# Performance work log

Hardware: AMD Instinct MI355X
Metric: run time of the kernel (lower is better)

## Reference

```python
import jax, jax.numpy as jnp
import numpy as np

B, S, D, H, EXPAND = 4, 2048, 256, 4, 4
DH = D // H
EPS = 1e-3  # keras BatchNormalization default epsilon
NEG = -1e9  # keras Softmax masking constant


def setup_inputs() -> dict:
    key = jax.random.key(0)
    ks = jax.random.split(key, 8)
    x = jax.random.normal(ks[0], (B, S, D), dtype=jnp.float32)
    mask = jax.random.randint(ks[1], (B, S), 0, 2) > 0
    mask = mask.at[:, 0].set(True)  # ensure each row has a valid token
    sc = 1.0 / np.sqrt(D)
    return {
        "x": x,
        "mask": mask,
        "bn1_gamma": jnp.ones((D,), jnp.float32),
        "bn1_beta": jnp.zeros((D,), jnp.float32),
        "bn1_mean": jax.random.normal(ks[2], (D,), jnp.float32) * 0.1,
        "bn1_var": jnp.ones((D,), jnp.float32),
        "qkv_w": jax.random.normal(ks[3], (D, 3 * D), jnp.float32) * sc,
        "proj_w": jax.random.normal(ks[4], (D, D), jnp.float32) * sc,
        "bn2_gamma": jnp.ones((D,), jnp.float32),
        "bn2_beta": jnp.zeros((D,), jnp.float32),
        "bn2_mean": jax.random.normal(ks[5], (D,), jnp.float32) * 0.1,
        "bn2_var": jnp.ones((D,), jnp.float32),
        "w1": jax.random.normal(ks[6], (D, EXPAND * D), jnp.float32) * sc,
        "w2": jax.random.normal(ks[7], (EXPAND * D, D), jnp.float32) * (sc / 2.0),
    }


def _bn(x, gamma, beta, mean, var):
    # inference-mode BatchNormalization over the channel axis
    return (x - mean) * jax.lax.rsqrt(var + EPS) * gamma + beta


def reference(x, mask, bn1_gamma, bn1_beta, bn1_mean, bn1_var, qkv_w, proj_w,
              bn2_gamma, bn2_beta, bn2_mean, bn2_var, w1, w2):
    scale = D ** (-0.5)
    # --- attention sub-block ---
    skip = x
    h = _bn(x, bn1_gamma, bn1_beta, bn1_mean, bn1_var)
    qkv = h @ qkv_w                                    # [B,S,3D]
    qkv = qkv.reshape(B, S, H, 3 * DH).transpose(0, 2, 1, 3)  # [B,H,S,3dh]
    q, k, v = qkv[..., :DH], qkv[..., DH:2 * DH], qkv[..., 2 * DH:]
    scores = jnp.einsum('bhqd,bhkd->bhqk', q, k) * scale      # [B,H,S,S]
    scores = scores + jnp.where(mask[:, None, None, :], 0.0, NEG)
    attn = jax.nn.softmax(scores, axis=-1)
    o = jnp.einsum('bhqk,bhkd->bhqd', attn, v)                # [B,H,S,dh]
    o = o.transpose(0, 2, 1, 3).reshape(B, S, D) @ proj_w
    x = o + skip
    # --- FFN sub-block ---
    skip = x
    h = _bn(x, bn2_gamma, bn2_beta, bn2_mean, bn2_var)
    h = jax.nn.swish(h @ w1)                                  # [B,S,4D]
    h = h @ w2
    return h + skip
```

## Files before the change

kernel.cpp:

```cpp
#include <hip/hip_runtime.h>
#include <math.h>

#define S_ 2048
#define D_ 256
#define B_ 4
#define H_ 4

typedef __attribute__((ext_vector_type(8))) short  bh8;
typedef __attribute__((ext_vector_type(4))) float  fx4;
typedef __attribute__((ext_vector_type(4))) unsigned short us4;
typedef __attribute__((ext_vector_type(4))) unsigned int   ux4;

__device__ inline unsigned short bf16r(float f) {
    unsigned int u = __builtin_bit_cast(unsigned int, f);
    return (unsigned short)((u + 0x7FFFu + ((u >> 16) & 1u)) >> 16);
}
__device__ inline unsigned int cvtpk(float a, float b) {
    unsigned int r;
    asm("v_cvt_pk_bf16_f32 %0, %1, %2" : "=v"(r) : "v"(a), "v"(b));
    return r;
}
__device__ inline float vexp2(float x) {
    float r;
    asm volatile("v_exp_f32 %0, %1\n\ts_nop 1" : "=v"(r) : "v"(x));
    return r;
}
__device__ inline void gl_lds16(const unsigned short* g, unsigned short* l) {
    __builtin_amdgcn_global_load_lds(
        (const __attribute__((address_space(1))) unsigned int*)g,
        (__attribute__((address_space(3))) unsigned int*)l, 16, 0, 0);
}
#define DRAIN_BARRIER() asm volatile("s_waitcnt vmcnt(0)\n\ts_barrier" ::: "memory")

__global__ __launch_bounds__(256) void prep_all_k(
    const float* __restrict__ qkv_w, const float* __restrict__ proj_w,
    const float* __restrict__ w1,    const float* __restrict__ w2,
    unsigned short* __restrict__ qkv_wt, unsigned short* __restrict__ proj_wt,
    unsigned short* __restrict__ w1t,    unsigned short* __restrict__ w2t,
    const float* __restrict__ x,
    const float* __restrict__ g1, const float* __restrict__ b1,
    const float* __restrict__ m1, const float* __restrict__ v1,
    unsigned short* __restrict__ xb,
    const int* __restrict__ mask, float* __restrict__ maskf)
{
    const int bidx = blockIdx.x;
    if (bidx < 768) {
        const float* W; unsigned short* Wt; int K, N, u0;
        if (bidx < 192)      { W = qkv_w;  Wt = qkv_wt;  K = 256;  N = 768;  u0 = bidx * 256; }
        else if (bidx < 256) { W = proj_w; Wt = proj_wt; K = 256;  N = 256;  u0 = (bidx - 192) * 256; }
        else if (bidx < 512) { W = w1;     Wt = w1t;     K = 256;  N = 1024; u0 = (bidx - 256) * 256; }
        else                 { W = w2;     Wt = w2t;     K = 1024; N = 256;  u0 = (bidx - 512) * 256; }
        const int u = u0 + threadIdx.x;
        const int k4 = u / N, n = u % N;
        us4 tv;
        #pragma unroll
        for (int j = 0; j < 4; ++j) tv[j] = bf16r(W[(size_t)(k4 * 4 + j) * N + n]);
        *(us4*)&Wt[(size_t)n * K + k4 * 4] = tv;
    } else if (bidx < 2816) {
        const int i = (bidx - 768) * 256 + threadIdx.x;
        const int c4 = (i & 63) * 4;
        float4 xv = *(const float4*)&x[(size_t)i * 4];
        float vv[4] = {xv.x, xv.y, xv.z, xv.w};
        us4 tv;
        #pragma unroll
        for (int j = 0; j < 4; ++j) {
            int c = c4 + j;
            float s = g1[c] * rsqrtf(v1[c] + 1e-3f);
            tv[j] = bf16r(vv[j] * s + (b1[c] - m1[c] * s));
        }
        *(us4*)&xb[(size_t)i * 4] = tv;
    } else {
        const int i = (bidx - 2816) * 256 + threadIdx.x;
        maskf[i] = mask[i] ? 0.0f : -1e9f;
    }
}

template<int BM, int E>
__global__ __launch_bounds__(256) void gemm_mfma_k(
    const unsigned short* __restrict__ A, const unsigned short* __restrict__ Wt,
    int N, int K,
    const float* __restrict__ res, float* __restrict__ outf,
    unsigned short* __restrict__ outb, unsigned short* __restrict__ kf_o,
    unsigned short* __restrict__ vf_o,
    const float* __restrict__ g2, const float* __restrict__ b2,
    const float* __restrict__ m2, const float* __restrict__ v2)
{
    constexpr int MI = BM / 32;
    constexpr int LA = BM / 32;
    __shared__ unsigned short Asb[2][BM * 64];
    __shared__ unsigned short Bsb[2][128 * 64];

    const int n0 = blockIdx.x * 128, m0 = blockIdx.y * BM;
    const int t = threadIdx.x, w = t >> 6, l = t & 63;
    const int qi = l & 15, g = l >> 4;
    const int wm = w >> 1, wn = w & 1;
    const int lr = l >> 3, lc = (l & 7) * 8;

    fx4 acc[MI][4];
    #pragma unroll
    for (int mi = 0; mi < MI; ++mi)
        #pragma unroll
        for (int ni = 0; ni < 4; ++ni) acc[mi][ni] = (fx4){0.f, 0.f, 0.f, 0.f};

    const int NT = K / 64;

#define STAGE(P, KT) {                                                        \
    const int kb = (KT) * 64;                                                 \
    _Pragma("unroll")                                                         \
    for (int i = 0; i < LA; ++i) {                                            \
        int r0 = (w * LA + i) * 8;                                            \
        gl_lds16(A + (size_t)(m0 + r0 + lr) * K + kb + lc, &Asb[P][r0 * 64]); \
    }                                                                         \
    _Pragma("unroll")                                                         \
    for (int i = 0; i < 4; ++i) {                                             \
        int r0 = (w * 4 + i) * 8;                                             \
        gl_lds16(Wt + (size_t)(n0 + r0 + lr) * K + kb + lc, &Bsb[P][r0 * 64]);\
    } }

    STAGE(0, 0);
    DRAIN_BARRIER();
    int p = 0;
    for (int kt = 0; kt < NT; ++kt) {
        if (kt + 1 < NT) STAGE(p ^ 1, kt + 1);
        #pragma unroll
        for (int kk = 0; kk < 2; ++kk) {
            bh8 af[MI], bf[4];
            #pragma unroll
            for (int mi = 0; mi < MI; ++mi)
                af[mi] = *(const bh8*)&Asb[p][(wm * (BM / 2) + mi * 16 + qi) * 64
                                             + kk * 32 + g * 8];
            #pragma unroll
            for (int ni = 0; ni < 4; ++ni)
                bf[ni] = *(const bh8*)&Bsb[p][(wn * 64 + ni * 16 + qi) * 64
                                             + kk * 32 + g * 8];
            #pragma unroll
            for (int mi = 0; mi < MI; ++mi)
                #pragma unroll
                for (int ni = 0; ni < 4; ++ni)
                    acc[mi][ni] = __builtin_amdgcn_mfma_f32_16x16x32_bf16(
                        af[mi], bf[ni], acc[mi][ni], 0, 0, 0);
        }
        DRAIN_BARRIER();
        p ^= 1;
    }
#undef STAGE

    const int mbase = m0 + wm * (BM / 2);
    #pragma unroll
    for (int ni = 0; ni < 4; ++ni) {
        const int nf = n0 + wn * 64 + ni * 16;
        if (E == 0) {
            const int h = nf / 192, rem = nf % 192;
            const int region = rem / 64;
            const int c = rem % 64 + qi;
            #pragma unroll
            for (int mi = 0; mi < MI; ++mi) {
                #pragma unroll
                for (int r = 0; r < 4; ++r) {
                    const int m = mbase + mi * 16 + g * 4 + r;
                    const int s = m & 2047;
                    const size_t bh = (size_t)((m >> 11) * 4 + h);
                    float a = acc[mi][ni][r];
                    if (region < 2) {
                        size_t off = (((bh * 128 + (s >> 4)) * 2 + (c >> 5)) * 64
                                      + ((c >> 3) & 3) * 16 + (s & 15)) * 8 + (c & 7);
                        if (region == 0)
                            outb[off] = bf16r(a * (0.0625f * 1.44269504f));
                        else
                            kf_o[off] = bf16r(a);
                    } else {
                        size_t off = ((((bh * 32 + (s >> 6)) * 4 + (c >> 4)) * 2
                                      + ((s >> 5) & 1)) * 64
                                      + ((s >> 3) & 3) * 16 + (c & 15)) * 8 + (s & 7);
                        vf_o[off] = bf16r(a);
                    }
                }
            }
        } else if (E == 1) {
            const int n = nf + qi;
            const float s2 = g2[n] * rsqrtf(v2[n] + 1e-3f);
            const float o2 = b2[n] - m2[n] * s2;
            #pragma unroll
            for (int mi = 0; mi < MI; ++mi) {
                #pragma unroll
                for (int r = 0; r < 4; ++r) {
                    const int m = mbase + mi * 16 + g * 4 + r;
                    const size_t idx = (size_t)m * N + n;
                    float rv = acc[mi][ni][r] + res[idx];
                    outf[idx] = rv;
                    outb[idx] = bf16r(rv * s2 + o2);
                }
            }
        } else if (E == 2) {
            const int n = nf + qi;
            #pragma unroll
            for (int mi = 0; mi < MI; ++mi) {
                #pragma unroll
                for (int r = 0; r < 4; ++r) {
                    const int m = mbase + mi * 16 + g * 4 + r;
                    float a = acc[mi][ni][r];
                    outb[(size_t)m * N + n] = bf16r(a / (1.0f + __expf(-a)));
                }
            }
        } else {
            const int n = nf + qi;
            #pragma unroll
            for (int mi = 0; mi < MI; ++mi) {
                #pragma unroll
                for (int r = 0; r < 4; ++r) {
                    const int m = mbase + mi * 16 + g * 4 + r;
                    const size_t idx = (size_t)m * N + n;
                    outf[idx] = acc[mi][ni][r] + res[idx];
                }
            }
        }
    }
}

__global__ __launch_bounds__(256) void attn_mfma_k(
    const unsigned short* __restrict__ qf,
    const unsigned short* __restrict__ kf,
    const unsigned short* __restrict__ vf,
    const float* __restrict__ maskf,
    unsigned short* __restrict__ ob)
{
    __shared__ fx4  Ol[2][64][4];
    __shared__ float Ll[2][64];

    const int bid = blockIdx.x;
    const int bh = bid & 15, qt = bid >> 4;
    const int b = bh >> 2, h = bh & 3;
    const int t = threadIdx.x;
    const int w = t >> 6, lane = t & 63;
    const int g = lane >> 4, qi = lane & 15;
    const int qsub = qt * 2 + (w & 1);
    const int khalf = w >> 1;

    bh8 qf0, qf1;
    {
        const unsigned short* qp =
            qf + (size_t)((bh * 128 + qsub) * 2) * 512 + lane * 8;
        qf0 = *(const bh8*)(qp);
        qf1 = *(const bh8*)(qp + 512);
    }

    fx4 o[4];
    #pragma unroll
    for (int dt = 0; dt < 4; ++dt) o[dt] = (fx4){0.f, 0.f, 0.f, 0.f};
    float lsum = 0.f;

    const unsigned short* kcur = kf + (size_t)bh * 131072 + khalf * 65536 + lane * 8;
    const unsigned short* vcur = vf + (size_t)bh * 131072 + khalf * 65536 + lane * 8;
    const float* mcur = maskf + b * 2048 + khalf * 1024 + g * 4;

    bh8 kfA[4][2], kfB[4][2], afA[4][2], afB[4][2];
    fx4 mvA[4], mvB[4];

#define LOADK(KF, MV) {                                                       \
    KF[0][0] = *(const bh8*)(kcur);        KF[0][1] = *(const bh8*)(kcur + 512);  \
    KF[1][0] = *(const bh8*)(kcur + 1024); KF[1][1] = *(const bh8*)(kcur + 1536); \
    KF[2][0] = *(const bh8*)(kcur + 2048); KF[2][1] = *(const bh8*)(kcur + 2560); \
    KF[3][0] = *(const bh8*)(kcur + 3072); KF[3][1] = *(const bh8*)(kcur + 3584); \
    MV[0] = *(const fx4*)(mcur);      MV[1] = *(const fx4*)(mcur + 16);       \
    MV[2] = *(const fx4*)(mcur + 32); MV[3] = *(const fx4*)(mcur + 48);       \
    kcur += 4096; mcur += 64; }

#define LOADV(AF) {                                                           \
    AF[0][0] = *(const bh8*)(vcur);        AF[0][1] = *(const bh8*)(vcur + 512);  \
    AF[1][0] = *(const bh8*)(vcur + 1024); AF[1][1] = *(const bh8*)(vcur + 1536); \
    AF[2][0] = *(const bh8*)(vcur + 2048); AF[2][1] = *(const bh8*)(vcur + 2560); \
    AF[3][0] = *(const bh8*)(vcur + 3072); AF[3][1] = *(const bh8*)(vcur + 3584); \
    vcur += 4096; }

#define PROCESS(KF, AF, MV) {                                                 \
    fx4 s[4];                                                                 \
    _Pragma("unroll")                                                         \
    for (int kt = 0; kt < 4; ++kt) {                                          \
        fx4 z = MV[kt];                                                       \
        z = __builtin_amdgcn_mfma_f32_16x16x32_bf16(KF[kt][0], qf0, z, 0, 0, 0); \
        z = __builtin_amdgcn_mfma_f32_16x16x32_bf16(KF[kt][1], qf1, z, 0, 0, 0); \
        s[kt] = z;                                                            \
    }                                                                         \
    unsigned int pkv[4][2];                                                   \
    _Pragma("unroll")                                                         \
    for (int kt = 0; kt < 4; ++kt) {                                          \
        float p0 = vexp2(s[kt][0]);                                           \
        float p1 = vexp2(s[kt][1]);                                           \
        float p2 = vexp2(s[kt][2]);                                           \
        float p3 = vexp2(s[kt][3]);                                           \
        lsum += (p0 + p1) + (p2 + p3);                                        \
        pkv[kt][0] = cvtpk(p0, p1);                                           \
        pkv[kt][1] = cvtpk(p2, p3);                                           \
    }                                                                         \
    _Pragma("unroll")                                                         \
    for (int c = 0; c < 2; ++c) {                                             \
        unsigned int bw[4];                                                   \
        _Pragma("unroll")                                                     \
        for (int wd = 0; wd < 4; ++wd) {                                      \
            int src = (2 * (g & 1) + (wd >> 1)) * 16 + qi;                    \
            unsigned int va = (unsigned int)__shfl((int)pkv[2 * c][wd & 1], src, 64);     \
            unsigned int vb = (unsigned int)__shfl((int)pkv[2 * c + 1][wd & 1], src, 64); \
            bw[wd] = (g >= 2) ? vb : va;                                      \
        }                                                                     \
        ux4 bwv = (ux4){bw[0], bw[1], bw[2], bw[3]};                          \
        bh8 bfrag = __builtin_bit_cast(bh8, bwv);                             \
        _Pragma("unroll")                                                     \
        for (int dt = 0; dt < 4; ++dt)                                        \
            o[dt] = __builtin_amdgcn_mfma_f32_16x16x32_bf16(                  \
                AF[dt][c], bfrag, o[dt], 0, 0, 0);                            \
    } }

    LOADK(kfA, mvA);
    LOADV(afA);
    for (int it = 0; it < 16; it += 2) {
        LOADK(kfB, mvB);
        LOADV(afB);
        PROCESS(kfA, afA, mvA);
        if (it + 2 < 16) {
            LOADK(kfA, mvA);
            LOADV(afA);
        }
        PROCESS(kfB, afB, mvB);
    }
#undef LOADK
#undef LOADV
#undef PROCESS

    const int pair = w & 1;
    if (w >= 2) {
        #pragma unroll
        for (int dt = 0; dt < 4; ++dt) Ol[pair][lane][dt] = o[dt];
        Ll[pair][lane] = lsum;
    }
    __syncthreads();
    if (w < 2) {
        lsum += Ll[pair][lane];
        #pragma unroll
        for (int dt = 0; dt < 4; ++dt) {
            fx4 ov = Ol[pair][lane][dt];
            o[dt][0] += ov[0]; o[dt][1] += ov[1];
            o[dt][2] += ov[2]; o[dt][3] += ov[3];
        }
        lsum += __shfl_xor(lsum, 16, 64);
        lsum += __shfl_xor(lsum, 32, 64);
        float inv = 1.0f / lsum;
        unsigned short* op =
            ob + (size_t)(b * 2048 + qsub * 16 + qi) * 256 + h * 64 + g * 4;
        #pragma unroll
        for (int dt = 0; dt < 4; ++dt) {
            us4 tv;
            #pragma unroll
            for (int r = 0; r < 4; ++r) tv[r] = bf16r(o[dt][r] * inv);
            *(us4*)(op + dt * 16) = tv;
        }
    }
}

extern "C" void kernel_launch(void* const* d_in, const int* in_sizes, int n_in,
                              void* d_out, int out_size, void* d_ws, size_t ws_size,
                              hipStream_t stream) {
    const float* x      = (const float*)d_in[0];
    const int*   mask   = (const int*)  d_in[1];
    const float* bn1_g  = (const float*)d_in[2];
    const float* bn1_b  = (const float*)d_in[3];
    const float* bn1_m  = (const float*)d_in[4];
    const float* bn1_v  = (const float*)d_in[5];
    const float* qkv_w  = (const float*)d_in[6];
    const float* proj_w = (const float*)d_in[7];
    const float* bn2_g  = (const float*)d_in[8];
    const float* bn2_b  = (const float*)d_in[9];
    const float* bn2_m  = (const float*)d_in[10];
    const float* bn2_v  = (const float*)d_in[11];
    const float* w1     = (const float*)d_in[12];
    const float* w2     = (const float*)d_in[13];
    float* out = (float*)d_out;

    char* w8 = (char*)d_ws;
    unsigned short* qkv_wt  = (unsigned short*)(w8 + 0);
    unsigned short* proj_wt = (unsigned short*)(w8 + 393216);
    unsigned short* w1t     = (unsigned short*)(w8 + 524288);
    unsigned short* w2t     = (unsigned short*)(w8 + 1048576);
    float*          maskf   = (float*)         (w8 + 1572864);
    unsigned short* xb      = (unsigned short*)(w8 + 2097152);
    float*          x2      = (float*)         (w8 + 6291456);
    unsigned short* x2nb    = (unsigned short*)(w8 + 14680064);
    unsigned short* qfrag   = (unsigned short*)(w8 + 18874368);
    unsigned short* kfrag   = (unsigned short*)(w8 + 23068672);
    unsigned short* vfrag   = (unsigned short*)(w8 + 27262976);
    unsigned short* ob      = (unsigned short*)(w8 + 31457280);
    unsigned short* h2b     = (unsigned short*)(w8 + 18874368);

    prep_all_k<<<2848, 256, 0, stream>>>(
        qkv_w, proj_w, w1, w2, qkv_wt, proj_wt, w1t, w2t,
        x, bn1_g, bn1_b, bn1_m, bn1_v, xb, mask, maskf);

    gemm_mfma_k<64, 0><<<dim3(6, 128), 256, 0, stream>>>(
        xb, qkv_wt, 768, 256, nullptr, nullptr, qfrag, kfrag, vfrag,
        nullptr, nullptr, nullptr, nullptr);

    attn_mfma_k<<<dim3(1024), 256, 0, stream>>>(qfrag, kfrag, vfrag, maskf, ob);

    gemm_mfma_k<32, 1><<<dim3(2, 256), 256, 0, stream>>>(
        ob, proj_wt, 256, 256, x, x2, x2nb, nullptr, nullptr,
        bn2_g, bn2_b, bn2_m, bn2_v);

    gemm_mfma_k<64, 2><<<dim3(8, 128), 256, 0, stream>>>(
        x2nb, w1t, 1024, 256, nullptr, nullptr, h2b, nullptr, nullptr,
        nullptr, nullptr, nullptr, nullptr);

    gemm_mfma_k<32, 3><<<dim3(2, 256), 256, 0, stream>>>(
        h2b, w2t, 256, 1024, x2, out, nullptr, nullptr, nullptr,
        nullptr, nullptr, nullptr, nullptr);
}
```

Baseline: 107.9 us.

## Process two query tiles per wave in attention to reuse K/V fragments

Each wave in the attention kernel now handles two 16-row query tiles instead of one, sharing each loaded K, V and mask fragment across both. The grid is halved from 1024 to 512 blocks. This halves global K/V traffic per query and gives each wave more independent MFMA work to hide latency. In exchange it raises register pressure and may lower occupancy, and fewer blocks may leave some compute units underfilled.

```diff
diff --git a/kernel.cpp b/kernel.cpp
--- a/kernel.cpp
+++ b/kernel.cpp
@@ -224,8 +224,8 @@
     const float* __restrict__ maskf,
     unsigned short* __restrict__ ob)
 {
-    __shared__ fx4  Ol[2][64][4];
-    __shared__ float Ll[2][64];
+    __shared__ fx4  Ol[2][64][8];
+    __shared__ float Ll[2][64][2];
 
     const int bid = blockIdx.x;
     const int bh = bid & 15, qt = bid >> 4;
@@ -233,21 +233,26 @@
     const int t = threadIdx.x;
     const int w = t >> 6, lane = t & 63;
     const int g = lane >> 4, qi = lane & 15;
-    const int qsub = qt * 2 + (w & 1);
+    const int qh = w & 1;
     const int khalf = w >> 1;
 
-    bh8 qf0, qf1;
+    bh8 qA0, qA1, qB0, qB1;
     {
         const unsigned short* qp =
-            qf + (size_t)((bh * 128 + qsub) * 2) * 512 + lane * 8;
-        qf0 = *(const bh8*)(qp);
-        qf1 = *(const bh8*)(qp + 512);
-    }
-
-    fx4 o[4];
+            qf + (size_t)(bh * 128 + qt * 4 + qh * 2) * 1024 + lane * 8;
+        qA0 = *(const bh8*)(qp);
+        qA1 = *(const bh8*)(qp + 512);
+        qB0 = *(const bh8*)(qp + 1024);
+        qB1 = *(const bh8*)(qp + 1536);
+    }
+
+    fx4 oA[4], oB[4];
     #pragma unroll
-    for (int dt = 0; dt < 4; ++dt) o[dt] = (fx4){0.f, 0.f, 0.f, 0.f};
-    float lsum = 0.f;
+    for (int dt = 0; dt < 4; ++dt) {
+        oA[dt] = (fx4){0.f, 0.f, 0.f, 0.f};
+        oB[dt] = (fx4){0.f, 0.f, 0.f, 0.f};
+    }
+    float lsA = 0.f, lsB = 0.f;
 
     const unsigned short* kcur = kf + (size_t)bh * 131072 + khalf * 65536 + lane * 8;
     const unsigned short* vcur = vf + (size_t)bh * 131072 + khalf * 65536 + lane * 8;
@@ -273,41 +278,56 @@
     vcur += 4096; }
 
 #define PROCESS(KF, AF, MV) {                                                 \
-    fx4 s[4];                                                                 \
+    fx4 sA[4], sB[4];                                                         \
     _Pragma("unroll")                                                         \
     for (int kt = 0; kt < 4; ++kt) {                                          \
-        fx4 z = MV[kt];                                                       \
-        z = __builtin_amdgcn_mfma_f32_16x16x32_bf16(KF[kt][0], qf0, z, 0, 0, 0); \
-        z = __builtin_amdgcn_mfma_f32_16x16x32_bf16(KF[kt][1], qf1, z, 0, 0, 0); \
-        s[kt] = z;                                                            \
+        fx4 zA = MV[kt];                                                      \
+        zA = __builtin_amdgcn_mfma_f32_16x16x32_bf16(KF[kt][0], qA0, zA, 0, 0, 0); \
+        zA = __builtin_amdgcn_mfma_f32_16x16x32_bf16(KF[kt][1], qA1, zA, 0, 0, 0); \
+        sA[kt] = zA;                                                          \
+        fx4 zB = MV[kt];                                                      \
+        zB = __builtin_amdgcn_mfma_f32_16x16x32_bf16(KF[kt][0], qB0, zB, 0, 0, 0); \
+        zB = __builtin_amdgcn_mfma_f32_16x16x32_bf16(KF[kt][1], qB1, zB, 0, 0, 0); \
+        sB[kt] = zB;                                                          \
     }                                                                         \
-    unsigned int pkv[4][2];                                                   \
+    unsigned int pkA[4][2], pkB[4][2];                                        \
     _Pragma("unroll")                                                         \
     for (int kt = 0; kt < 4; ++kt) {                                          \
-        float p0 = vexp2(s[kt][0]);                                           \
-        float p1 = vexp2(s[kt][1]);                                           \
-        float p2 = vexp2(s[kt][2]);                                           \
-        float p3 = vexp2(s[kt][3]);                                           \
-        lsum += (p0 + p1) + (p2 + p3);                                        \
-        pkv[kt][0] = cvtpk(p0, p1);                                           \
-        pkv[kt][1] = cvtpk(p2, p3);                                           \
+        float a0 = vexp2(sA[kt][0]);                                          \
+        float a1 = vexp2(sA[kt][1]);                                          \
+        float a2 = vexp2(sA[kt][2]);                                          \
+        float a3 = vexp2(sA[kt][3]);                                          \
+        lsA += (a0 + a1) + (a2 + a3);                                         \
+        pkA[kt][0] = cvtpk(a0, a1);                                           \
+        pkA[kt][1] = cvtpk(a2, a3);                                           \
+        float b0 = vexp2(sB[kt][0]);                                          \
+        float b1 = vexp2(sB[kt][1]);                                          \
+        float b2 = vexp2(sB[kt][2]);                                          \
+        float b3 = vexp2(sB[kt][3]);                                          \
+        lsB += (b0 + b1) + (b2 + b3);                                         \
+        pkB[kt][0] = cvtpk(b0, b1);                                           \
+        pkB[kt][1] = cvtpk(b2, b3);                                           \
     }                                                                         \
     _Pragma("unroll")                                                         \
     for (int c = 0; c < 2; ++c) {                                             \
-        unsigned int bw[4];                                                   \
+        unsigned int bwA[4], bwB[4];                                          \
         _Pragma("unroll")                                                     \
         for (int wd = 0; wd < 4; ++wd) {                                      \
             int src = (2 * (g & 1) + (wd >> 1)) * 16 + qi;                    \
-            unsigned int va = (unsigned int)__shfl((int)pkv[2 * c][wd & 1], src, 64);     \
-            unsigned int vb = (unsigned int)__shfl((int)pkv[2 * c + 1][wd & 1], src, 64); \
-            bw[wd] = (g >= 2) ? vb : va;                                      \
+            unsigned int vaA = (unsigned int)__shfl((int)pkA[2 * c][wd & 1], src, 64);     \
+            unsigned int vbA = (unsigned int)__shfl((int)pkA[2 * c + 1][wd & 1], src, 64); \
+            bwA[wd] = (g >= 2) ? vbA : vaA;                                   \
+            unsigned int vaB = (unsigned int)__shfl((int)pkB[2 * c][wd & 1], src, 64);     \
+            unsigned int vbB = (unsigned int)__shfl((int)pkB[2 * c + 1][wd & 1], src, 64); \
+            bwB[wd] = (g >= 2) ? vbB : vaB;                                   \
         }                                                                     \
-        ux4 bwv = (ux4){bw[0], bw[1], bw[2], bw[3]};                          \
-        bh8 bfrag = __builtin_bit_cast(bh8, bwv);                             \
+        bh8 bfA = __builtin_bit_cast(bh8, (ux4){bwA[0], bwA[1], bwA[2], bwA[3]}); \
+        bh8 bfB = __builtin_bit_cast(bh8, (ux4){bwB[0], bwB[1], bwB[2], bwB[3]}); \
         _Pragma("unroll")                                                     \
-        for (int dt = 0; dt < 4; ++dt)                                        \
-            o[dt] = __builtin_amdgcn_mfma_f32_16x16x32_bf16(                  \
-                AF[dt][c], bfrag, o[dt], 0, 0, 0);                            \
+        for (int dt = 0; dt < 4; ++dt) {                                      \
+            oA[dt] = __builtin_amdgcn_mfma_f32_16x16x32_bf16(AF[dt][c], bfA, oA[dt], 0, 0, 0); \
+            oB[dt] = __builtin_amdgcn_mfma_f32_16x16x32_bf16(AF[dt][c], bfB, oB[dt], 0, 0, 0); \
+        }                                                                     \
     } }
 
     LOADK(kfA, mvA);
@@ -326,32 +346,44 @@
 #undef LOADV
 #undef PROCESS
 
-    const int pair = w & 1;
+    const int slot = w & 1;
     if (w >= 2) {
         #pragma unroll
-        for (int dt = 0; dt < 4; ++dt) Ol[pair][lane][dt] = o[dt];
-        Ll[pair][lane] = lsum;
+        for (int dt = 0; dt < 4; ++dt) {
+            Ol[slot][lane][dt]     = oA[dt];
+            Ol[slot][lane][4 + dt] = oB[dt];
+        }
+        Ll[slot][lane][0] = lsA;
+        Ll[slot][lane][1] = lsB;
     }
     __syncthreads();
     if (w < 2) {
-        lsum += Ll[pair][lane];
+        lsA += Ll[slot][lane][0];
+        lsB += Ll[slot][lane][1];
         #pragma unroll
         for (int dt = 0; dt < 4; ++dt) {
-            fx4 ov = Ol[pair][lane][dt];
-            o[dt][0] += ov[0]; o[dt][1] += ov[1];
-            o[dt][2] += ov[2]; o[dt][3] += ov[3];
-        }
-        lsum += __shfl_xor(lsum, 16, 64);
-        lsum += __shfl_xor(lsum, 32, 64);
-        float inv = 1.0f / lsum;
-        unsigned short* op =
-            ob + (size_t)(b * 2048 + qsub * 16 + qi) * 256 + h * 64 + g * 4;
+            fx4 pa = Ol[slot][lane][dt], pb = Ol[slot][lane][4 + dt];
+            oA[dt][0] += pa[0]; oA[dt][1] += pa[1]; oA[dt][2] += pa[2]; oA[dt][3] += pa[3];
+            oB[dt][0] += pb[0]; oB[dt][1] += pb[1]; oB[dt][2] += pb[2]; oB[dt][3] += pb[3];
+        }
+        lsA += __shfl_xor(lsA, 16, 64);
+        lsA += __shfl_xor(lsA, 32, 64);
+        lsB += __shfl_xor(lsB, 16, 64);
+        lsB += __shfl_xor(lsB, 32, 64);
+        float invA = 1.0f / lsA, invB = 1.0f / lsB;
+        unsigned short* opA =
+            ob + (size_t)(b * 2048 + qt * 64 + qh * 32 + qi) * 256 + h * 64 + g * 4;
+        unsigned short* opB = opA + 16 * 256;
         #pragma unroll
         for (int dt = 0; dt < 4; ++dt) {
-            us4 tv;
-            #pragma unroll
-            for (int r = 0; r < 4; ++r) tv[r] = bf16r(o[dt][r] * inv);
-            *(us4*)(op + dt * 16) = tv;
+            us4 ta, tb;
+            #pragma unroll
+            for (int r = 0; r < 4; ++r) {
+                ta[r] = bf16r(oA[dt][r] * invA);
+                tb[r] = bf16r(oB[dt][r] * invB);
+            }
+            *(us4*)(opA + dt * 16) = ta;
+            *(us4*)(opB + dt * 16) = tb;
         }
     }
 }
@@ -398,7 +430,7 @@
         xb, qkv_wt, 768, 256, nullptr, nullptr, qfrag, kfrag, vfrag,
         nullptr, nullptr, nullptr, nullptr);
 
-    attn_mfma_k<<<dim3(1024), 256, 0, stream>>>(qfrag, kfrag, vfrag, maskf, ob);
+    attn_mfma_k<<<dim3(512), 256, 0, stream>>>(qfrag, kfrag, vfrag, maskf, ob);
 
     gemm_mfma_k<32, 1><<<dim3(2, 256), 256, 0, stream>>>(
         ob, proj_wt, 256, 256, x, x2, x2nb, nullptr, nullptr,
```

New measurement: 102.9 us. 1.05x faster.
